# Kernel optimization log

Hardware: AMD Instinct MI355X
Metric: run time of the kernel (lower is better)

The kernel has to match this reference:

```python
import jax, jax.numpy as jnp
import numpy as np


def setup_inputs() -> dict:
    key = jax.random.key(0)
    k1, k2 = jax.random.split(key)
    B, S, D, O = 4, 4096, 2048, 2048
    inputs = jax.random.normal(k1, (B, S, D), dtype=jnp.float32)
    # truncated-normal-like init with stddev 1/sqrt(fan_in)
    w = jax.random.normal(k2, (D, O), dtype=jnp.float32) * (1.0 / np.sqrt(D))
    b = jnp.zeros((O,), dtype=jnp.float32)
    return {"inputs": inputs, "w": w, "b": b}


def reference(inputs, w, b):
    # logsumexp-semiring linear layer (basis=None path):
    #   out = log(exp(inputs - max_in) @ exp(w - max_w)) + max_in + max_w + b
    max_inputs = jnp.max(inputs)          # global scalar max for stabilization
    max_w = jnp.max(w)
    exp_inputs = jnp.exp(inputs - max_inputs)   # [B, S, D]
    exp_w = jnp.exp(w - max_w)                  # [D, O]
    out = jnp.log(jnp.dot(exp_inputs, exp_w))   # [B, S, O]
    out = out + (max_inputs + max_w)
    out = out + b                               # broadcast bias over [B, S, O]
    return out
```

## Files before the change

### kernel.cpp

```cpp
#include <hip/hip_runtime.h>

typedef int   i32x4v __attribute__((ext_vector_type(4)));
typedef int   i32x8v __attribute__((ext_vector_type(8)));
typedef float f32x16 __attribute__((ext_vector_type(16)));

#define GLOBAL_AS(p) ((const __attribute__((address_space(1))) void*)(p))
#define LDS_AS(p)    ((__attribute__((address_space(3))) void*)(p))
#define BAR()     __builtin_amdgcn_s_barrier()
#define VMCNT(n)  asm volatile("s_waitcnt vmcnt(" #n ")" ::: "memory")

__device__ inline int fp4_code(float v) {
  return (v > 0.25f) + (v > 0.75f) + (v > 1.25f) + (v > 1.75f) +
         (v > 2.5f) + (v > 3.5f) + (v > 5.0f);
}

__global__ void expcvt_a4_kernel(const float* __restrict__ x,
                                 unsigned char* __restrict__ A4,
                                 unsigned char* __restrict__ SAt,
                                 int M, int K) {
  const int NKB = K >> 5;
  const int t = blockIdx.x * blockDim.x + threadIdx.x;
  const int m = t / NKB, kb = t - m * NKB;
  if (m >= M) return;
  const float4* xs4 = (const float4*)(x + (size_t)m * K + kb * 32);
  float a[32];
  float bm = -3.0e38f;
#pragma unroll
  for (int j = 0; j < 8; ++j) {
    float4 v = xs4[j];
    a[4 * j] = v.x; a[4 * j + 1] = v.y; a[4 * j + 2] = v.z; a[4 * j + 3] = v.w;
    bm = fmaxf(bm, fmaxf(fmaxf(v.x, v.y), fmaxf(v.z, v.w)));
  }
  int e = (int)ceilf(bm * 1.44269504f - 2.58496250f);
  e = min(127, max(-126, e));
  SAt[(size_t)kb * M + ((m >> 7) << 7) + ((m & 31) << 2) + ((m >> 5) & 3)] =
      (unsigned char)(e + 127);
  uint4 u;
  unsigned d[4];
#pragma unroll
  for (int g = 0; g < 4; ++g) {
    unsigned acc = 0;
#pragma unroll
    for (int j = 0; j < 8; ++j) {
      float v = exp2f(a[g * 8 + j] * 1.44269504f - (float)e);
      acc |= (unsigned)fp4_code(v) << (4 * j);
    }
    d[g] = acc;
  }
  u.x = d[0]; u.y = d[1]; u.z = d[2]; u.w = d[3];
  *(uint4*)(A4 + (size_t)m * (K >> 1) + kb * 16) = u;
}

__global__ void expcvt_wt4_kernel(const float* __restrict__ w,
                                  unsigned char* __restrict__ Bt4,
                                  unsigned char* __restrict__ SBt,
                                  int D, int O) {
  __shared__ float tile[32][33];
  int c0 = blockIdx.x * 32;
  int r0 = blockIdx.y * 32;
  int tx = threadIdx.x;
  int ty = threadIdx.y;
#pragma unroll
  for (int j = 0; j < 4; ++j) {
    int r = r0 + ty + j * 8;
    tile[ty + j * 8][tx] = __expf(w[(size_t)r * O + c0 + tx]);
  }
  __syncthreads();
  if (ty == 0) {
    const int n = c0 + tx;
    float bm = 0.0f;
#pragma unroll
    for (int d = 0; d < 32; ++d) bm = fmaxf(bm, tile[d][tx]);
    int e = (int)ceilf(__log2f(bm) - 2.58496250f);
    e = min(127, max(-126, e));
    SBt[(size_t)(r0 >> 5) * O + ((n >> 7) << 7) + ((n & 31) << 2) +
        ((n >> 5) & 3)] = (unsigned char)(e + 127);
    const float inv = exp2f(-(float)e);
    uint4 u;
    unsigned d4[4];
#pragma unroll
    for (int g = 0; g < 4; ++g) {
      unsigned acc = 0;
#pragma unroll
      for (int j = 0; j < 8; ++j)
        acc |= (unsigned)fp4_code(tile[g * 8 + j][tx] * inv) << (4 * j);
      d4[g] = acc;
    }
    u.x = d4[0]; u.y = d4[1]; u.z = d4[2]; u.w = d4[3];
    *(uint4*)(Bt4 + (size_t)n * (D >> 1) + (r0 >> 1)) = u;
  }
}


#define MFMA4(MB, NB, AV, BV, SAv, SBv)                                      \
  acc[MB][NB] = __builtin_amdgcn_mfma_scale_f32_32x32x64_f8f6f4(             \
      AV, BV, acc[MB][NB], 4, 4, 0, SAv, 0, SBv);

__global__ __launch_bounds__(256, 4) void gemm_mx4d_kernel(
    const unsigned char* __restrict__ A4, const unsigned char* __restrict__ Bt4,
    const unsigned char* __restrict__ SAt, const unsigned char* __restrict__ SBt,
    const float* __restrict__ bias, float* __restrict__ out,
    int M, int N, int K) {
  __shared__ char lds[34816];

  const int tid = threadIdx.x;
  const int wid = tid >> 6, lane = tid & 63;
  const int wr = wid >> 1, wc = wid & 1;
  const int l31 = lane & 31, lk = lane >> 5;
  const int NTK = K >> 7;
  const size_t Kb = (size_t)K >> 1;

  const int cpx = gridDim.x >> 3;
  const int v   = (blockIdx.x & 7) * cpx + (blockIdx.x >> 3);
  const int nbn = N >> 7;
  const int bm  = v / nbn, bn = v % nbn;
  const int brow = bm << 7, bcol = bn << 7;

  const int swz = ((l31 & 6) << 3) ^ (l31 & 16);
  const int cR0 = (lk << 5) ^ swz;

  const char* gA[2];
  const char* gB[2];
#pragma unroll
  for (int i = 0; i < 2; ++i) {
    const int o = i * 4096 + tid * 16, row = o >> 6;
    const int sg = (((row & 6) << 3) ^ (row & 16)) >> 4;
    const int gl = ((o >> 4) & 3) ^ sg;
    const int gs = ((gl & 1) << 1) | (gl >> 1);
    gA[i] = (const char*)A4 + (size_t)(brow + row) * Kb + (gs << 4);
    gB[i] = (const char*)Bt4 + (size_t)(bcol + row) * Kb + (gs << 4);
  }
  const char* gS;
  size_t sstep;
  if (wid < 2) {
    gS = (const char*)SAt + ((size_t)(lane >> 5) + 2 * wid) * M + brow + l31 * 4;
    sstep = 4 * (size_t)M;
  } else {
    gS = (const char*)SBt + ((size_t)(lane >> 5) + 2 * (wid - 2)) * N + bcol +
         l31 * 4;
    sstep = 4 * (size_t)N;
  }

  auto STAGE = [&](int t, char* base) {
    const int tt = (t < NTK) ? t : NTK - 1;
    const int koff = tt << 6;
#pragma unroll
    for (int i = 0; i < 2; ++i) {
      __builtin_amdgcn_global_load_lds(GLOBAL_AS(gA[i] + koff),
          LDS_AS(base + i * 4096 + wid * 1024), 16, 0, 0);
      __builtin_amdgcn_global_load_lds(GLOBAL_AS(gB[i] + koff),
          LDS_AS(base + 8192 + i * 4096 + wid * 1024), 16, 0, 0);
    }
    __builtin_amdgcn_global_load_lds(GLOBAL_AS(gS + (size_t)tt * sstep),
        LDS_AS(base + 16384 + wid * 256 + lane * 4), 4, 0, 0);
  };

  f32x16 acc[2][2];
#pragma unroll
  for (int m = 0; m < 2; ++m)
#pragma unroll
    for (int n = 0; n < 2; ++n) acc[m][n] = (f32x16)0.0f;

  const int shA = wr << 4;
  const int shB = wc << 4;

  auto COMPUTE = [&](const char* base) {
    const char* bA = base + wr * 4096;
    const char* bB = base + 8192 + wc * 4096;
#pragma unroll
    for (int h = 0; h < 2; ++h) {
      const int ch = cR0 ^ (h << 4);
      i32x8v a8[2], b8[2];
#pragma unroll
      for (int mb = 0; mb < 2; ++mb) {
        i32x4v f = *(const i32x4v*)(bA + (mb * 32 + l31) * 64 + ch);
        a8[mb] = __builtin_shufflevector(f, f, 0, 1, 2, 3, -1, -1, -1, -1);
      }
#pragma unroll
      for (int nb = 0; nb < 2; ++nb) {
        i32x4v f = *(const i32x4v*)(bB + (nb * 32 + l31) * 64 + ch);
        b8[nb] = __builtin_shufflevector(f, f, 0, 1, 2, 3, -1, -1, -1, -1);
      }
      const int kb2 = 2 * h + lk;
      const int saw = *(const int*)(base + 16384 + kb2 * 128 + l31 * 4);
      const int sbw = *(const int*)(base + 16896 + kb2 * 128 + l31 * 4);
      const int sA0 = (saw >> shA) & 0xFF, sA1 = (saw >> (shA + 8)) & 0xFF;
      const int sB0 = (sbw >> shB) & 0xFF, sB1 = (sbw >> (shB + 8)) & 0xFF;
      MFMA4(0, 0, a8[0], b8[0], sA0, sB0)
      MFMA4(1, 0, a8[1], b8[0], sA1, sB0)
      MFMA4(0, 1, a8[0], b8[1], sA0, sB1)
      MFMA4(1, 1, a8[1], b8[1], sA1, sB1)
    }
  };

  char* const L0 = lds;
  char* const L1 = lds + 17408;

  STAGE(0, L0);

  for (int j = 0; j < (NTK >> 1); ++j) {
    STAGE(2 * j + 1, L1);
    VMCNT(5);
    BAR();
    COMPUTE(L0);
    BAR();
    STAGE(2 * j + 2, L0);
    VMCNT(5);
    BAR();
    COMPUTE(L1);
    BAR();
  }

  VMCNT(0);

  const int col0 = bcol + wc * 64 + l31;
  const int row0 = brow + wr * 64 + lk * 4;
  const float bv0 = bias[col0], bv1 = bias[col0 + 32];
#pragma unroll
  for (int mb = 0; mb < 2; ++mb) {
#pragma unroll
    for (int rg = 0; rg < 16; ++rg) {
      const int row = row0 + mb * 32 + (rg & 3) + 8 * (rg >> 2);
      const size_t ro = (size_t)row * N + col0;
      __builtin_nontemporal_store(__logf(acc[mb][0][rg]) + bv0, &out[ro]);
      __builtin_nontemporal_store(__logf(acc[mb][1][rg]) + bv1, &out[ro + 32]);
    }
  }
}

extern "C" void kernel_launch(void* const* d_in, const int* in_sizes, int n_in,
                              void* d_out, int out_size, void* d_ws, size_t ws_size,
                              hipStream_t stream) {
  const float* inputs = (const float*)d_in[0];
  const float* w      = (const float*)d_in[1];
  const float* bias   = (const float*)d_in[2];
  float* out = (float*)d_out;

  const int O = in_sizes[2];
  const int D = in_sizes[1] / O;
  const size_t MD = (size_t)in_sizes[0];
  const int M = (int)(MD / (size_t)D);

  unsigned char* ws  = (unsigned char*)d_ws;
  unsigned char* A4  = ws;
  unsigned char* Bt4 = ws + MD / 2;
  unsigned char* SAt = Bt4 + (size_t)O * D / 2;
  unsigned char* SBt = SAt + MD / 32;

  const int nthr = (int)((MD / 32 + 255) / 256);
  expcvt_a4_kernel<<<nthr, 256, 0, stream>>>(inputs, A4, SAt, M, D);

  dim3 tg(O / 32, D / 32);
  expcvt_wt4_kernel<<<tg, dim3(32, 8), 0, stream>>>(w, Bt4, SBt, D, O);

  dim3 grid((M / 128) * (O / 128));
  gemm_mx4d_kernel<<<grid, 256, 0, stream>>>(A4, Bt4, SAt, SBt, bias, out,
                                             M, O, D);
}
```

Measured before the change: 88.79 us.

## Load A fragments and scales directly to registers, stage only B in LDS

The GEMM kernel no longer stages the A tile and the scale bytes through LDS. Each wave loads its A fragments and scale words from global memory straight into registers, double-buffered one tile ahead. Only B is still staged through LDS, which halves the LDS footprint, and the MFMA section is wrapped in s_setprio. This cuts LDS traffic and footprint, but A is now read redundantly by the two waves that share rows, and the VMCNT accounting becomes more fragile.

New measurement: 126.6 us. 42.6% more time.

```diff
diff --git a/kernel.cpp b/kernel.cpp
--- a/kernel.cpp
+++ b/kernel.cpp
@@ -8,6 +8,8 @@
 #define LDS_AS(p)    ((__attribute__((address_space(3))) void*)(p))
 #define BAR()     __builtin_amdgcn_s_barrier()
 #define VMCNT(n)  asm volatile("s_waitcnt vmcnt(" #n ")" ::: "memory")
+#define SP1       __builtin_amdgcn_s_setprio(1);
+#define SP0       __builtin_amdgcn_s_setprio(0);
 
 __device__ inline int fp4_code(float v) {
   return (v > 0.25f) + (v > 0.75f) + (v > 1.25f) + (v > 1.75f) +
@@ -92,16 +94,63 @@
 }
 
 
+#define PAD8(f) __builtin_shufflevector(f, f, 0, 1, 2, 3, -1, -1, -1, -1)
 #define MFMA4(MB, NB, AV, BV, SAv, SBv)                                      \
   acc[MB][NB] = __builtin_amdgcn_mfma_scale_f32_32x32x64_f8f6f4(             \
       AV, BV, acc[MB][NB], 4, 4, 0, SAv, 0, SBv);
 
-__global__ __launch_bounds__(256, 4) void gemm_mx4d_kernel(
+#define SCALES(T, S0, S1, S2, S3)                                            \
+  {                                                                          \
+    const int tt = ((T) < NTK) ? (T) : NTK - 1;                              \
+    S0 = *(const int*)(pSA + (size_t)(tt * 4) * M);                          \
+    S1 = *(const int*)(pSA + (size_t)(tt * 4 + 2) * M);                      \
+    S2 = *(const int*)(pSB + (size_t)(tt * 4) * N);                          \
+    S3 = *(const int*)(pSB + (size_t)(tt * 4 + 2) * N);                      \
+  }
+
+#define AFRAGS(T)                                                            \
+  {                                                                          \
+    const int tt = ((T) < NTK) ? (T) : NTK - 1;                              \
+    const int ko = tt << 6;                                                  \
+    aF00 = *(const i32x4v*)(aB0 + ko);                                       \
+    aF01 = *(const i32x4v*)(aB0 + ko + 32);                                  \
+    aF10 = *(const i32x4v*)(aB1 + ko);                                       \
+    aF11 = *(const i32x4v*)(aB1 + ko + 32);                                  \
+  }
+
+#define COMPUTE(BASE, SAW0, SAW1, SBW0, SBW1)                                \
+  {                                                                          \
+    const char* bB = (BASE) + wc * 4096;                                     \
+    {                                                                        \
+      const int ch = cR0;                                                    \
+      i32x4v f0 = *(const i32x4v*)(bB + l31 * 64 + ch);                      \
+      i32x4v f1 = *(const i32x4v*)(bB + (32 + l31) * 64 + ch);               \
+      const int sA0 = ((SAW0) >> shA) & 0xFF, sA1 = ((SAW0) >> (shA + 8)) & 0xFF; \
+      const int sB0 = ((SBW0) >> shB) & 0xFF, sB1 = ((SBW0) >> (shB + 8)) & 0xFF; \
+      MFMA4(0, 0, PAD8(aF00), PAD8(f0), sA0, sB0)                            \
+      MFMA4(1, 0, PAD8(aF10), PAD8(f0), sA1, sB0)                            \
+      MFMA4(0, 1, PAD8(aF00), PAD8(f1), sA0, sB1)                            \
+      MFMA4(1, 1, PAD8(aF10), PAD8(f1), sA1, sB1)                            \
+    }                                                                        \
+    {                                                                        \
+      const int ch = cR0 ^ 16;                                               \
+      i32x4v f0 = *(const i32x4v*)(bB + l31 * 64 + ch);                      \
+      i32x4v f1 = *(const i32x4v*)(bB + (32 + l31) * 64 + ch);               \
+      const int sA0 = ((SAW1) >> shA) & 0xFF, sA1 = ((SAW1) >> (shA + 8)) & 0xFF; \
+      const int sB0 = ((SBW1) >> shB) & 0xFF, sB1 = ((SBW1) >> (shB + 8)) & 0xFF; \
+      MFMA4(0, 0, PAD8(aF01), PAD8(f0), sA0, sB0)                            \
+      MFMA4(1, 0, PAD8(aF11), PAD8(f0), sA1, sB0)                            \
+      MFMA4(0, 1, PAD8(aF01), PAD8(f1), sA0, sB1)                            \
+      MFMA4(1, 1, PAD8(aF11), PAD8(f1), sA1, sB1)                            \
+    }                                                                        \
+  }
+
+__global__ __launch_bounds__(256, 4) void gemm_mx4e_kernel(
     const unsigned char* __restrict__ A4, const unsigned char* __restrict__ Bt4,
     const unsigned char* __restrict__ SAt, const unsigned char* __restrict__ SBt,
     const float* __restrict__ bias, float* __restrict__ out,
     int M, int N, int K) {
-  __shared__ char lds[34816];
+  __shared__ char lds[16384];
 
   const int tid = threadIdx.x;
   const int wid = tid >> 6, lane = tid & 63;
@@ -119,7 +168,6 @@
   const int swz = ((l31 & 6) << 3) ^ (l31 & 16);
   const int cR0 = (lk << 5) ^ swz;
 
-  const char* gA[2];
   const char* gB[2];
 #pragma unroll
   for (int i = 0; i < 2; ++i) {
@@ -127,32 +175,22 @@
     const int sg = (((row & 6) << 3) ^ (row & 16)) >> 4;
     const int gl = ((o >> 4) & 3) ^ sg;
     const int gs = ((gl & 1) << 1) | (gl >> 1);
-    gA[i] = (const char*)A4 + (size_t)(brow + row) * Kb + (gs << 4);
     gB[i] = (const char*)Bt4 + (size_t)(bcol + row) * Kb + (gs << 4);
   }
-  const char* gS;
-  size_t sstep;
-  if (wid < 2) {
-    gS = (const char*)SAt + ((size_t)(lane >> 5) + 2 * wid) * M + brow + l31 * 4;
-    sstep = 4 * (size_t)M;
-  } else {
-    gS = (const char*)SBt + ((size_t)(lane >> 5) + 2 * (wid - 2)) * N + bcol +
-         l31 * 4;
-    sstep = 4 * (size_t)N;
-  }
-
-  auto STAGE = [&](int t, char* base) {
+
+  const char* aB0 = (const char*)A4 + (size_t)(brow + wr * 64 + l31) * Kb + lk * 16;
+  const char* aB1 = aB0 + (size_t)32 * Kb;
+
+  const char* pSA = (const char*)SAt + (size_t)lk * M + brow + l31 * 4;
+  const char* pSB = (const char*)SBt + (size_t)lk * N + bcol + l31 * 4;
+
+  auto STAGE_B = [&](int t, char* base) {
     const int tt = (t < NTK) ? t : NTK - 1;
     const int koff = tt << 6;
 #pragma unroll
-    for (int i = 0; i < 2; ++i) {
-      __builtin_amdgcn_global_load_lds(GLOBAL_AS(gA[i] + koff),
+    for (int i = 0; i < 2; ++i)
+      __builtin_amdgcn_global_load_lds(GLOBAL_AS(gB[i] + koff),
           LDS_AS(base + i * 4096 + wid * 1024), 16, 0, 0);
-      __builtin_amdgcn_global_load_lds(GLOBAL_AS(gB[i] + koff),
-          LDS_AS(base + 8192 + i * 4096 + wid * 1024), 16, 0, 0);
-    }
-    __builtin_amdgcn_global_load_lds(GLOBAL_AS(gS + (size_t)tt * sstep),
-        LDS_AS(base + 16384 + wid * 256 + lane * 4), 4, 0, 0);
   };
 
   f32x16 acc[2][2];
@@ -164,50 +202,31 @@
   const int shA = wr << 4;
   const int shB = wc << 4;
 
-  auto COMPUTE = [&](const char* base) {
-    const char* bA = base + wr * 4096;
-    const char* bB = base + 8192 + wc * 4096;
-#pragma unroll
-    for (int h = 0; h < 2; ++h) {
-      const int ch = cR0 ^ (h << 4);
-      i32x8v a8[2], b8[2];
-#pragma unroll
-      for (int mb = 0; mb < 2; ++mb) {
-        i32x4v f = *(const i32x4v*)(bA + (mb * 32 + l31) * 64 + ch);
-        a8[mb] = __builtin_shufflevector(f, f, 0, 1, 2, 3, -1, -1, -1, -1);
-      }
-#pragma unroll
-      for (int nb = 0; nb < 2; ++nb) {
-        i32x4v f = *(const i32x4v*)(bB + (nb * 32 + l31) * 64 + ch);
-        b8[nb] = __builtin_shufflevector(f, f, 0, 1, 2, 3, -1, -1, -1, -1);
-      }
-      const int kb2 = 2 * h + lk;
-      const int saw = *(const int*)(base + 16384 + kb2 * 128 + l31 * 4);
-      const int sbw = *(const int*)(base + 16896 + kb2 * 128 + l31 * 4);
-      const int sA0 = (saw >> shA) & 0xFF, sA1 = (saw >> (shA + 8)) & 0xFF;
-      const int sB0 = (sbw >> shB) & 0xFF, sB1 = (sbw >> (shB + 8)) & 0xFF;
-      MFMA4(0, 0, a8[0], b8[0], sA0, sB0)
-      MFMA4(1, 0, a8[1], b8[0], sA1, sB0)
-      MFMA4(0, 1, a8[0], b8[1], sA0, sB1)
-      MFMA4(1, 1, a8[1], b8[1], sA1, sB1)
-    }
-  };
-
   char* const L0 = lds;
-  char* const L1 = lds + 17408;
-
-  STAGE(0, L0);
+  char* const L1 = lds + 8192;
+
+  i32x4v aF00, aF01, aF10, aF11;
+  int sE0, sE1, sE2, sE3, sO0, sO1, sO2, sO3;
+
+  STAGE_B(0, L0);
+  SCALES(0, sE0, sE1, sE2, sE3);
+  AFRAGS(0);
 
   for (int j = 0; j < (NTK >> 1); ++j) {
-    STAGE(2 * j + 1, L1);
-    VMCNT(5);
-    BAR();
-    COMPUTE(L0);
-    BAR();
-    STAGE(2 * j + 2, L0);
-    VMCNT(5);
-    BAR();
-    COMPUTE(L1);
+    const int t0 = 2 * j;
+    STAGE_B(t0 + 1, L1);
+    SCALES(t0 + 1, sO0, sO1, sO2, sO3);
+    VMCNT(6);
+    BAR();
+    SP1 COMPUTE(L0, sE0, sE1, sE2, sE3) SP0
+    AFRAGS(t0 + 1);
+    BAR();
+    STAGE_B(t0 + 2, L0);
+    SCALES(t0 + 2, sE0, sE1, sE2, sE3);
+    VMCNT(6);
+    BAR();
+    SP1 COMPUTE(L1, sO0, sO1, sO2, sO3) SP0
+    AFRAGS(t0 + 2);
     BAR();
   }
 
@@ -254,6 +273,6 @@
   expcvt_wt4_kernel<<<tg, dim3(32, 8), 0, stream>>>(w, Bt4, SBt, D, O);
 
   dim3 grid((M / 128) * (O / 128));
-  gemm_mx4d_kernel<<<grid, 256, 0, stream>>>(A4, Bt4, SAt, SBt, bias, out,
+  gemm_mx4e_kernel<<<grid, 256, 0, stream>>>(A4, Bt4, SAt, SBt, bias, out,
                                              M, O, D);
 }
```
